# Performance work log

Hardware: AMD Instinct MI355X
Metric: run time of the kernel (lower is better)

The kernel has to match this reference:

```python
import jax, jax.numpy as jnp
import numpy as np

B = 4096
D = 1024
NUM_CLASSES = 100
TEMPERATURE = 0.5
EPS = 1e-12  # matches F.normalize default eps


def setup_inputs() -> dict:
    key = jax.random.key(0)
    k1, k2, k3 = jax.random.split(key, 3)
    emb_i = jax.random.normal(k1, (B, D), dtype=jnp.float32)
    emb_j = jax.random.normal(k2, (B, D), dtype=jnp.float32)
    labels = jax.random.randint(k3, (B,), 0, NUM_CLASSES, dtype=jnp.int32)
    return {"emb_i": emb_i, "emb_j": emb_j, "labels": labels}


def _l2_normalize(x):
    # F.normalize(x, dim=1): x / max(||x||, eps)
    n = jnp.sqrt(jnp.sum(x * x, axis=1, keepdims=True))
    return x / jnp.maximum(n, EPS)


def reference(emb_i, emb_j, labels):
    z_i = _l2_normalize(emb_i)
    z_j = _l2_normalize(emb_j)
    reps = jnp.concatenate([z_i, z_j], axis=0)          # [2B, D]
    # cosine similarity of already-unit vectors == dot product (GEMM instead
    # of the O(N^2 D) broadcasted elementwise form in the torch code)
    sim = jnp.einsum("nd,md->nm", reps, reps)           # [2B, 2B]

    n2 = 2 * B
    neg_mask = 1.0 - jnp.eye(n2, dtype=sim.dtype)       # exclude self-pairs
    label_t = jnp.concatenate([labels, labels], axis=0)  # [2B]
    ws = (label_t[:, None] == label_t[None, :]).astype(sim.dtype) * neg_mask

    e = jnp.exp(sim / TEMPERATURE)                      # [2B, 2B]
    nominator = jnp.sum(ws * e, axis=1)                 # [2B]
    denominator = jnp.sum(neg_mask * e, axis=1)         # [2B]
    loss_partial = -jnp.log(nominator / denominator)
    return jnp.sum(loss_partial) / (2 * B)
```

## Files before the change

kernel.cpp:

```cpp
#include <hip/hip_runtime.h>
#include <hip/hip_bf16.h>
#include <hip/hip_fp8.h>


#define BHALF 4096
#define N2 8192
#define DK 1024
#define DKB 512
#define TILE 128
#define BKB 64
#define NTILE 64
#define NBLK 2080

typedef __attribute__((ext_vector_type(16))) float f32x16;
typedef __attribute__((ext_vector_type(4))) int v4i;
typedef __attribute__((ext_vector_type(8))) int v8i;
typedef unsigned char u8;
typedef unsigned short u16;

#define EXP_SCALE4 0.0028177637517362566f
#define UNIT_SCALE 0x7f7f7f7f

#define WAITVM(n) asm volatile("s_waitcnt vmcnt(" #n ")" ::: "memory")
#define BAR()     asm volatile("s_barrier" ::: "memory")

static __device__ __forceinline__ float fexp2(float x) {
    float r;
    asm("v_exp_f32 %0, %1\n\ts_nop 1" : "=v"(r) : "v"(x));
    return r;
}

static __device__ __forceinline__ unsigned nib4(float x) {
    unsigned s = (__builtin_bit_cast(unsigned, x) >> 31) << 3;
    float a = fminf(fabsf(x), 6.0f);
    unsigned c;
    if (a < 2.0f)      c = (unsigned)lrintf(a * 2.0f);
    else if (a < 4.0f) c = (unsigned)lrintf(a) + 2u;
    else               c = (a < 5.0f) ? 6u : 7u;
    return s | c;
}

__global__ __launch_bounds__(256) void normalize_kernel(
    const float* __restrict__ emb_i, const float* __restrict__ emb_j,
    u16* __restrict__ reps, float* __restrict__ out) {
    int idx = blockIdx.x * 256 + threadIdx.x;
    if (idx == 0) out[0] = 0.0f;
    int r = blockIdx.x * 4 + (threadIdx.x >> 6);
    int lane = threadIdx.x & 63;
    const float* src = (r < BHALF) ? (emb_i + (size_t)r * DK)
                                   : (emb_j + (size_t)(r - BHALF) * DK);
    const float4* srcv = (const float4*)src;
    float4 v[4];
    float s = 0.f;
#pragma unroll
    for (int k = 0; k < 4; ++k) {
        v[k] = srcv[k * 64 + lane];
        s += v[k].x * v[k].x + v[k].y * v[k].y +
             v[k].z * v[k].z + v[k].w * v[k].w;
    }
#pragma unroll
    for (int m = 1; m <= 32; m <<= 1) s += __shfl_xor(s, m, 64);
    float scale = 32.0f / fmaxf(sqrtf(s), 1e-12f);
    u16* dst = reps + (size_t)r * 256;
#pragma unroll
    for (int k = 0; k < 4; ++k) {
        unsigned p = nib4(v[k].x * scale) |
                     (nib4(v[k].y * scale) << 4) |
                     (nib4(v[k].z * scale) << 8) |
                     (nib4(v[k].w * scale) << 12);
        dst[k * 64 + lane] = (u16)p;
    }
}

__global__ __launch_bounds__(256, 3) void gemm_loss_kernel(
    const u8* __restrict__ reps, const int* __restrict__ labels,
    float2* __restrict__ parts) {
    __shared__ __align__(16) u8 A_s[3][TILE * BKB];
    __shared__ __align__(16) u8 B_s[3][TILE * BKB];
    __shared__ float2 red2[2][128];

    int g = blockIdx.x;
    int rem = (g & 7) * 260 + (g >> 3);
    int bi = 0;
    while (rem >= NTILE - bi) { rem -= NTILE - bi; ++bi; }
    int bj = bi + rem;
    int rowBase = bi * TILE;
    int colBase = bj * TILE;

    int tid = threadIdx.x;
    int w = tid >> 6;
    int lane = tid & 63;
    int wm = w >> 1, wn = w & 1;
    int hk = lane >> 5;
    int l31 = lane & 31;

    ((float*)red2)[tid] = 0.0f;
    ((float*)red2)[tid + 256] = 0.0f;

    f32x16 acc[2][2];
#pragma unroll
    for (int i = 0; i < 2; ++i)
#pragma unroll
        for (int j = 0; j < 2; ++j)
#pragma unroll
            for (int r = 0; r < 16; ++r) acc[i][j][r] = 0.0f;

    int srow = lane >> 2;
    int sbg = (lane & 3) ^ ((srow ^ (srow >> 2)) & 3);
    const u8* gA = reps + (size_t)(rowBase + w * 32 + srow) * DKB + sbg * 16;
    const u8* gB = reps + (size_t)(colBase + w * 32 + srow) * DKB + sbg * 16;

    int rswz = (l31 ^ (l31 >> 2)) & 3;
    unsigned aOff[2][2], bOff[2][2];
#pragma unroll
    for (int i = 0; i < 2; ++i) {
#pragma unroll
        for (int ks = 0; ks < 2; ++ks) {
            int ra = (wm * 64 + i * 32 + l31) * BKB;
            aOff[i][ks] = ra + (((ks * 2 + hk) ^ rswz) << 4);
            int rb = (wn * 64 + i * 32 + l31) * BKB;
            bOff[i][ks] = rb + (((ks * 2 + hk) ^ rswz) << 4);
        }
    }

#define STAGE(buf, kt)                                                       \
    {                                                                        \
        _Pragma("unroll")                                                    \
        for (int c = 0; c < 2; ++c) {                                        \
            int chunk = 2 * w + c;                                           \
            __builtin_amdgcn_global_load_lds(                                \
                (const __attribute__((address_space(1))) void*)              \
                    (gA + (size_t)c * 16 * DKB + (kt) * BKB),                \
                (__attribute__((address_space(3))) void*)                    \
                    &A_s[buf][chunk * 1024], 16, 0, 0);                      \
            __builtin_amdgcn_global_load_lds(                                \
                (const __attribute__((address_space(1))) void*)              \
                    (gB + (size_t)c * 16 * DKB + (kt) * BKB),                \
                (__attribute__((address_space(3))) void*)                    \
                    &B_s[buf][chunk * 1024], 16, 0, 0);                      \
        }                                                                    \
    }
#define COMPUTE(buf)                                                         \
    {                                                                        \
        _Pragma("unroll")                                                    \
        for (int ks = 0; ks < 2; ++ks) {                                     \
            v8i aF[2], bF[2];                                                \
            _Pragma("unroll")                                                \
            for (int i = 0; i < 2; ++i) {                                    \
                v4i a4 = *(const v4i*)&A_s[buf][aOff[i][ks]];                \
                aF[i] = __builtin_shufflevector(a4, a4, 0,1,2,3,-1,-1,-1,-1);\
                v4i b4 = *(const v4i*)&B_s[buf][bOff[i][ks]];                \
                bF[i] = __builtin_shufflevector(b4, b4, 0,1,2,3,-1,-1,-1,-1);\
            }                                                                \
            __builtin_amdgcn_s_setprio(1);                                   \
            _Pragma("unroll")                                                \
            for (int i = 0; i < 2; ++i)                                      \
                _Pragma("unroll")                                            \
                for (int j = 0; j < 2; ++j)                                  \
                    acc[i][j] =                                              \
                        __builtin_amdgcn_mfma_scale_f32_32x32x64_f8f6f4(     \
                            aF[i], bF[j], acc[i][j], 4, 4,                   \
                            0, UNIT_SCALE, 0, UNIT_SCALE);                   \
            __builtin_amdgcn_s_setprio(0);                                   \
        }                                                                    \
    }

    STAGE(0, 0)
    STAGE(1, 1)
    WAITVM(4); BAR(); STAGE(2, 2) COMPUTE(0)
    WAITVM(4); BAR(); STAGE(0, 3) COMPUTE(1)
    WAITVM(4); BAR(); STAGE(1, 4) COMPUTE(2)
    WAITVM(4); BAR(); STAGE(2, 5) COMPUTE(0)
    WAITVM(4); BAR(); STAGE(0, 6) COMPUTE(1)
    WAITVM(4); BAR(); STAGE(1, 7) COMPUTE(2)
    WAITVM(4); BAR();             COMPUTE(0)
    WAITVM(0); BAR();             COMPUTE(1)
#undef STAGE
#undef COMPUTE

    bool offd = (bi != bj);
    int lc[2], gcol[2];
#pragma unroll
    for (int j = 0; j < 2; ++j) {
        gcol[j] = colBase + wn * 64 + j * 32 + l31;
        lc[j] = labels[gcol[j] & (BHALF - 1)];
    }

    float colD[2] = {0.f, 0.f}, colN[2] = {0.f, 0.f};
#pragma unroll
    for (int i = 0; i < 2; ++i) {
        float v[32];
#pragma unroll
        for (int reg = 0; reg < 16; ++reg) {
            int rowIn = (reg & 3) + 8 * (reg >> 2) + 4 * hk;
            int grow = rowBase + wm * 64 + i * 32 + rowIn;
            int labr = labels[grow & (BHALF - 1)];
            float rD = 0.f, rN = 0.f;
#pragma unroll
            for (int j = 0; j < 2; ++j) {
                float e = fexp2(acc[i][j][reg] * EXP_SCALE4);
                if (grow == gcol[j]) e = 0.f;
                bool m = (lc[j] == labr);
                rD += e; if (m) rN += e;
                colD[j] += e; if (m) colN[j] += e;
            }
            v[reg] = rD;
            v[16 + reg] = rN;
        }
#pragma unroll
        for (int step = 0; step < 5; ++step) {
            const int m = 16 >> step;
            const int h = 16 >> step;
            bool up = (l31 & m) != 0;
#pragma unroll
            for (int k = 0; k < h; ++k) {
                float sV = up ? v[k] : v[k + h];
                float kV = up ? v[k + h] : v[k];
                v[k] = kV + __shfl_xor(sV, m, 64);
            }
        }
        {
            int reg = l31 & 15;
            int rowOff = wm * 64 + i * 32 +
                         ((reg & 3) + 8 * (reg >> 2) + 4 * hk);
            float* cell = (l31 & 16) ? &red2[0][rowOff].x
                                     : &red2[0][rowOff].y;
            atomicAdd(cell, v[0]);
        }
    }
    if (offd) {
#pragma unroll
        for (int j = 0; j < 2; ++j) {
            float cd = colD[j] + __shfl_xor(colD[j], 32, 64);
            float cn = colN[j] + __shfl_xor(colN[j], 32, 64);
            if (hk == 0) {
                int colOff = wn * 64 + j * 32 + l31;
                atomicAdd(&red2[1][colOff].x, cn);
                atomicAdd(&red2[1][colOff].y, cd);
            }
        }
    }
    __syncthreads();
    if (tid < 128) {
        parts[(size_t)bj * N2 + rowBase + tid] = red2[0][tid];
    } else if (offd) {
        parts[(size_t)bi * N2 + colBase + tid - 128] = red2[1][tid - 128];
    }
}

__global__ __launch_bounds__(256) void finalize_kernel(
    const float2* __restrict__ parts, float* __restrict__ out) {
    int row = blockIdx.x * 256 + threadIdx.x;
    int t = threadIdx.x;
    float n = 0.f, d = 0.f;
#pragma unroll 8
    for (int s = 0; s < NTILE; ++s) {
        float2 p = parts[(size_t)s * N2 + row];
        n += p.x;
        d += p.y;
    }
    float sv = logf(d) - logf(n);
#pragma unroll
    for (int m = 1; m <= 32; m <<= 1) sv += __shfl_xor(sv, m, 64);
    __shared__ float red[4];
    if ((t & 63) == 0) red[t >> 6] = sv;
    __syncthreads();
    if (t == 0)
        atomicAdd(out, (red[0] + red[1] + red[2] + red[3]) / (float)N2);
}

extern "C" void kernel_launch(void* const* d_in, const int* in_sizes, int n_in,
                              void* d_out, int out_size, void* d_ws, size_t ws_size,
                              hipStream_t stream) {
    const float* emb_i = (const float*)d_in[0];
    const float* emb_j = (const float*)d_in[1];
    const int* labels  = (const int*)d_in[2];
    float* out = (float*)d_out;

    char* ws = (char*)d_ws;
    u8* reps     = (u8*)ws;
    float2* parts = (float2*)(ws + (size_t)N2 * DKB);

    normalize_kernel<<<2048, 256, 0, stream>>>(emb_i, emb_j, (u16*)reps, out);
    gemm_loss_kernel<<<NBLK, 256, 0, stream>>>(reps, labels, parts);
    finalize_kernel<<<(N2 + 255) / 256, 256, 0, stream>>>(parts, out);
}
```

Measured before the change: 124.2 us.

## Switch GEMM-loss to single-wave 64x64 tiles with barrier-free double buffering

```diff
diff --git a/kernel.cpp b/kernel.cpp
--- a/kernel.cpp
+++ b/kernel.cpp
@@ -7,10 +7,11 @@
 #define N2 8192
 #define DK 1024
 #define DKB 512
-#define TILE 128
+#define TILE 64
 #define BKB 64
-#define NTILE 64
-#define NBLK 2080
+#define NTILE 128
+#define NBLK 8256
+#define CPX 1032
 
 typedef __attribute__((ext_vector_type(16))) float f32x16;
 typedef __attribute__((ext_vector_type(4))) int v4i;
@@ -22,7 +23,7 @@
 #define UNIT_SCALE 0x7f7f7f7f
 
 #define WAITVM(n) asm volatile("s_waitcnt vmcnt(" #n ")" ::: "memory")
-#define BAR()     asm volatile("s_barrier" ::: "memory")
+#define LGKM0()   asm volatile("s_waitcnt lgkmcnt(0)" ::: "memory")
 
 static __device__ __forceinline__ float fexp2(float x) {
     float r;
@@ -72,31 +73,24 @@
     }
 }
 
-__global__ __launch_bounds__(256, 3) void gemm_loss_kernel(
+__global__ __launch_bounds__(64, 4) void gemm_loss_kernel(
     const u8* __restrict__ reps, const int* __restrict__ labels,
     float2* __restrict__ parts) {
-    __shared__ __align__(16) u8 A_s[3][TILE * BKB];
-    __shared__ __align__(16) u8 B_s[3][TILE * BKB];
-    __shared__ float2 red2[2][128];
+    __shared__ __align__(16) u8 A_s[2][TILE * BKB];
+    __shared__ __align__(16) u8 B_s[2][TILE * BKB];
 
     int g = blockIdx.x;
-    int rem = (g & 7) * 260 + (g >> 3);
+    int rem = (g & 7) * CPX + (g >> 3);
     int bi = 0;
     while (rem >= NTILE - bi) { rem -= NTILE - bi; ++bi; }
     int bj = bi + rem;
     int rowBase = bi * TILE;
     int colBase = bj * TILE;
 
-    int tid = threadIdx.x;
-    int w = tid >> 6;
-    int lane = tid & 63;
-    int wm = w >> 1, wn = w & 1;
+    int lane = threadIdx.x;
     int hk = lane >> 5;
     int l31 = lane & 31;
 
-    ((float*)red2)[tid] = 0.0f;
-    ((float*)red2)[tid + 256] = 0.0f;
-
     f32x16 acc[2][2];
 #pragma unroll
     for (int i = 0; i < 2; ++i)
@@ -107,8 +101,8 @@
 
     int srow = lane >> 2;
     int sbg = (lane & 3) ^ ((srow ^ (srow >> 2)) & 3);
-    const u8* gA = reps + (size_t)(rowBase + w * 32 + srow) * DKB + sbg * 16;
-    const u8* gB = reps + (size_t)(colBase + w * 32 + srow) * DKB + sbg * 16;
+    const u8* gA = reps + (size_t)(rowBase + srow) * DKB + sbg * 16;
+    const u8* gB = reps + (size_t)(colBase + srow) * DKB + sbg * 16;
 
     int rswz = (l31 ^ (l31 >> 2)) & 3;
     unsigned aOff[2][2], bOff[2][2];
@@ -116,28 +110,25 @@
     for (int i = 0; i < 2; ++i) {
 #pragma unroll
         for (int ks = 0; ks < 2; ++ks) {
-            int ra = (wm * 64 + i * 32 + l31) * BKB;
-            aOff[i][ks] = ra + (((ks * 2 + hk) ^ rswz) << 4);
-            int rb = (wn * 64 + i * 32 + l31) * BKB;
-            bOff[i][ks] = rb + (((ks * 2 + hk) ^ rswz) << 4);
+            aOff[i][ks] = (i * 32 + l31) * BKB + (((ks * 2 + hk) ^ rswz) << 4);
+            bOff[i][ks] = (i * 32 + l31) * BKB + (((ks * 2 + hk) ^ rswz) << 4);
         }
     }
 
 #define STAGE(buf, kt)                                                       \
     {                                                                        \
         _Pragma("unroll")                                                    \
-        for (int c = 0; c < 2; ++c) {                                        \
-            int chunk = 2 * w + c;                                           \
+        for (int c = 0; c < 4; ++c) {                                        \
             __builtin_amdgcn_global_load_lds(                                \
                 (const __attribute__((address_space(1))) void*)              \
                     (gA + (size_t)c * 16 * DKB + (kt) * BKB),                \
                 (__attribute__((address_space(3))) void*)                    \
-                    &A_s[buf][chunk * 1024], 16, 0, 0);                      \
+                    &A_s[buf][c * 1024], 16, 0, 0);                          \
             __builtin_amdgcn_global_load_lds(                                \
                 (const __attribute__((address_space(1))) void*)              \
                     (gB + (size_t)c * 16 * DKB + (kt) * BKB),                \
                 (__attribute__((address_space(3))) void*)                    \
-                    &B_s[buf][chunk * 1024], 16, 0, 0);                      \
+                    &B_s[buf][c * 1024], 16, 0, 0);                          \
         }                                                                    \
     }
 #define COMPUTE(buf)                                                         \
@@ -152,7 +143,6 @@
                 v4i b4 = *(const v4i*)&B_s[buf][bOff[i][ks]];                \
                 bF[i] = __builtin_shufflevector(b4, b4, 0,1,2,3,-1,-1,-1,-1);\
             }                                                                \
-            __builtin_amdgcn_s_setprio(1);                                   \
             _Pragma("unroll")                                                \
             for (int i = 0; i < 2; ++i)                                      \
                 _Pragma("unroll")                                            \
@@ -161,20 +151,19 @@
                         __builtin_amdgcn_mfma_scale_f32_32x32x64_f8f6f4(     \
                             aF[i], bF[j], acc[i][j], 4, 4,                   \
                             0, UNIT_SCALE, 0, UNIT_SCALE);                   \
-            __builtin_amdgcn_s_setprio(0);                                   \
         }                                                                    \
     }
 
     STAGE(0, 0)
     STAGE(1, 1)
-    WAITVM(4); BAR(); STAGE(2, 2) COMPUTE(0)
-    WAITVM(4); BAR(); STAGE(0, 3) COMPUTE(1)
-    WAITVM(4); BAR(); STAGE(1, 4) COMPUTE(2)
-    WAITVM(4); BAR(); STAGE(2, 5) COMPUTE(0)
-    WAITVM(4); BAR(); STAGE(0, 6) COMPUTE(1)
-    WAITVM(4); BAR(); STAGE(1, 7) COMPUTE(2)
-    WAITVM(4); BAR();             COMPUTE(0)
-    WAITVM(0); BAR();             COMPUTE(1)
+    WAITVM(8); COMPUTE(0) LGKM0(); STAGE(0, 2)
+    WAITVM(8); COMPUTE(1) LGKM0(); STAGE(1, 3)
+    WAITVM(8); COMPUTE(0) LGKM0(); STAGE(0, 4)
+    WAITVM(8); COMPUTE(1) LGKM0(); STAGE(1, 5)
+    WAITVM(8); COMPUTE(0) LGKM0(); STAGE(0, 6)
+    WAITVM(8); COMPUTE(1) LGKM0(); STAGE(1, 7)
+    WAITVM(8); COMPUTE(0)
+    WAITVM(0); COMPUTE(1)
 #undef STAGE
 #undef COMPUTE
 
@@ -182,7 +171,7 @@
     int lc[2], gcol[2];
 #pragma unroll
     for (int j = 0; j < 2; ++j) {
-        gcol[j] = colBase + wn * 64 + j * 32 + l31;
+        gcol[j] = colBase + j * 32 + l31;
         lc[j] = labels[gcol[j] & (BHALF - 1)];
     }
 
@@ -193,7 +182,7 @@
 #pragma unroll
         for (int reg = 0; reg < 16; ++reg) {
             int rowIn = (reg & 3) + 8 * (reg >> 2) + 4 * hk;
-            int grow = rowBase + wm * 64 + i * 32 + rowIn;
+            int grow = rowBase + i * 32 + rowIn;
             int labr = labels[grow & (BHALF - 1)];
             float rD = 0.f, rN = 0.f;
 #pragma unroll
@@ -219,13 +208,13 @@
                 v[k] = kV + __shfl_xor(sV, m, 64);
             }
         }
-        {
-            int reg = l31 & 15;
-            int rowOff = wm * 64 + i * 32 +
-                         ((reg & 3) + 8 * (reg >> 2) + 4 * hk);
-            float* cell = (l31 & 16) ? &red2[0][rowOff].x
-                                     : &red2[0][rowOff].y;
-            atomicAdd(cell, v[0]);
+        float nOther = __shfl_xor(v[0], 16, 64);
+        if (l31 < 16) {
+            int reg = l31;
+            int grow = rowBase + i * 32 +
+                       ((reg & 3) + 8 * (reg >> 2) + 4 * hk);
+            float2 p; p.x = nOther; p.y = v[0];
+            parts[(size_t)bj * N2 + grow] = p;
         }
     }
     if (offd) {
@@ -234,17 +223,10 @@
             float cd = colD[j] + __shfl_xor(colD[j], 32, 64);
             float cn = colN[j] + __shfl_xor(colN[j], 32, 64);
             if (hk == 0) {
-                int colOff = wn * 64 + j * 32 + l31;
-                atomicAdd(&red2[1][colOff].x, cn);
-                atomicAdd(&red2[1][colOff].y, cd);
+                float2 p; p.x = cn; p.y = cd;
+                parts[(size_t)bi * N2 + gcol[j]] = p;
             }
         }
-    }
-    __syncthreads();
-    if (tid < 128) {
-        parts[(size_t)bj * N2 + rowBase + tid] = red2[0][tid];
-    } else if (offd) {
-        parts[(size_t)bi * N2 + colBase + tid - 128] = red2[1][tid - 128];
     }
 }
 
@@ -259,7 +241,7 @@
         n += p.x;
         d += p.y;
     }
-    float sv = logf(d) - logf(n);
+    float sv = __logf(d) - __logf(n);
 #pragma unroll
     for (int m = 1; m <= 32; m <<= 1) sv += __shfl_xor(sv, m, 64);
     __shared__ float red[4];
@@ -282,6 +264,6 @@
     float2* parts = (float2*)(ws + (size_t)N2 * DKB);
 
     normalize_kernel<<<2048, 256, 0, stream>>>(emb_i, emb_j, (u16*)reps, out);
-    gemm_loss_kernel<<<NBLK, 256, 0, stream>>>(reps, labels, parts);
+    gemm_loss_kernel<<<NBLK, 64, 0, stream>>>(reps, labels, parts);
     finalize_kernel<<<(N2 + 255) / 256, 256, 0, stream>>>(parts, out);
 }
```

After: 136.9 us. +10.2%, slower.
